# Performance work log

Measured on AMD Instinct MI355X. Metric: run time of the kernel, lower is better.

The kernel has to match this reference:

```python
import jax, jax.numpy as jnp
import numpy as np

D = 1024      # atrybuty (d_model)
H = 16        # kanaly (heads)
DH = D // H   # head dim
B, T = 4, 2048
EPS = 1e-5


def setup_inputs() -> dict:
    key = jax.random.key(0)
    ks = jax.random.split(key, 16)
    s = 0.02
    return {
        "x":  jax.random.normal(ks[0], (B, T, D), jnp.float32),
        "wq": jax.random.normal(ks[1], (D, D), jnp.float32) * s,
        "wk": jax.random.normal(ks[2], (D, D), jnp.float32) * s,
        "wv": jax.random.normal(ks[3], (D, D), jnp.float32) * s,
        "wp": jax.random.normal(ks[4], (D, D), jnp.float32) * s,
        "bp": jnp.zeros((D,), jnp.float32),
        "w1": jax.random.normal(ks[5], (D, 4 * D), jnp.float32) * s,
        "b1": jnp.zeros((4 * D,), jnp.float32),
        "w2": jax.random.normal(ks[6], (4 * D, D), jnp.float32) * s,
        "b2": jnp.zeros((D,), jnp.float32),
        "g1": jnp.ones((D,), jnp.float32),
        "be1": jnp.zeros((D,), jnp.float32),
        "g2": jnp.ones((D,), jnp.float32),
        "be2": jnp.zeros((D,), jnp.float32),
    }


def _layernorm(x, g, b):
    mu = jnp.mean(x, axis=-1, keepdims=True)
    var = jnp.mean(jnp.square(x - mu), axis=-1, keepdims=True)
    return (x - mu) * jax.lax.rsqrt(var + EPS) * g + b


def reference(x, wq, wk, wv, wp, bp, w1, b1, w2, b2, g1, be1, g2, be2):
    b, t, d = x.shape
    # --- self-attention on ln1(x) ---
    h = _layernorm(x, g1, be1)
    # per-head Linears are equivalent to one [D,D] projection split into heads
    q = (h @ wq).reshape(b, t, H, DH).transpose(0, 2, 1, 3)  # [B,H,T,Dh]
    k = (h @ wk).reshape(b, t, H, DH).transpose(0, 2, 1, 3)
    v = (h @ wv).reshape(b, t, H, DH).transpose(0, 2, 1, 3)
    # NOTE: original scales by full embed dim C, not head_dim
    scale = jnp.asarray(d, x.dtype) ** -0.5
    wei = jnp.einsum("bhqd,bhkd->bhqk", q, k) * scale
    causal = jnp.tril(jnp.ones((t, t), bool))
    wei = jnp.where(causal, wei, -jnp.inf)
    wei = jax.nn.softmax(wei, axis=-1)
    att = jnp.einsum("bhqk,bhkd->bhqd", wei, v)
    att = att.transpose(0, 2, 1, 3).reshape(b, t, d)
    x = x + att @ wp + bp
    # --- feedforward on ln2(x) ---
    h2 = _layernorm(x, g2, be2)
    x = x + jax.nn.relu(h2 @ w1 + b1) @ w2 + b2
    return x
```

## Files before the change

kernel.cpp:

```cpp
#include <hip/hip_runtime.h>
#include <hip/hip_bf16.h>
#include <stdint.h>

#define DM   1024
#define NH   16
#define DH   64
#define BATCH 4
#define SEQ  2048
#define MROWS (BATCH*SEQ)

typedef float f32x4 __attribute__((ext_vector_type(4)));
typedef __bf16 bf16x8 __attribute__((ext_vector_type(8)));
typedef short s16x4 __attribute__((ext_vector_type(4)));
typedef int   i32x2 __attribute__((ext_vector_type(2)));

#define QSCALE 0.045084220f

#define VM(n) asm volatile("s_waitcnt vmcnt(" #n ")" ::: "memory")
#define LGKM0 do { asm volatile("s_waitcnt lgkmcnt(0)" ::: "memory"); \
                   __builtin_amdgcn_sched_barrier(0); } while (0)

__device__ __forceinline__ short f2bs(float f) {
    __bf16 h = (__bf16)f;
    return __builtin_bit_cast(short, h);
}

__device__ __forceinline__ void gload_lds16(const void* g, void* l) {
    __builtin_amdgcn_global_load_lds(
        (__attribute__((address_space(1))) void*)(g),
        (__attribute__((address_space(3))) void*)(l), 16, 0, 0);
}

__device__ __forceinline__ void swz_xy(int ny, int& x, int& y) {
    const int bid = blockIdx.x;
    const int cpx = gridDim.x >> 3;
    const int wg  = (bid & 7) * cpx + (bid >> 3);
    x = wg / ny;
    y = wg % ny;
}

__global__ __launch_bounds__(256) void transpose_cvt_kernel(
    const float* __restrict__ w, short* __restrict__ wt, int K, int N)
{
    __shared__ short tile[64 * 65];
    const int k0 = blockIdx.x * 64, n0 = blockIdx.y * 64;
    const int t = threadIdx.x;
#pragma unroll
    for (int i = 0; i < 16; ++i) {
        int idx = i * 256 + t;
        int r = idx >> 6, c = idx & 63;
        tile[r * 65 + c] = f2bs(w[(size_t)(k0 + r) * N + n0 + c]);
    }
    __syncthreads();
#pragma unroll
    for (int i = 0; i < 16; ++i) {
        int idx = i * 256 + t;
        int r = idx >> 6, c = idx & 63;
        wt[(size_t)(n0 + r) * K + k0 + c] = tile[c * 65 + r];
    }
}

__global__ __launch_bounds__(256) void ln_kernel(
    const float* __restrict__ x, const float* __restrict__ g,
    const float* __restrict__ be, short* __restrict__ out)
{
    const int row = blockIdx.x, t = threadIdx.x;
    const float4 v = ((const float4*)(x + (size_t)row * DM))[t];
    float s  = v.x + v.y + v.z + v.w;
    float ss = v.x * v.x + v.y * v.y + v.z * v.z + v.w * v.w;
#pragma unroll
    for (int d = 1; d < 64; d <<= 1) {
        s  += __shfl_xor(s, d, 64);
        ss += __shfl_xor(ss, d, 64);
    }
    __shared__ float red[8];
    const int wid = t >> 6;
    if ((t & 63) == 0) { red[wid] = s; red[wid + 4] = ss; }
    __syncthreads();
    s  = red[0] + red[1] + red[2] + red[3];
    ss = red[4] + red[5] + red[6] + red[7];
    const float mu = s * (1.0f / DM);
    const float rs = rsqrtf(ss * (1.0f / DM) - mu * mu + 1e-5f);
    const float4 gg = ((const float4*)g)[t];
    const float4 bb = ((const float4*)be)[t];
    short4 o;
    o.x = f2bs((v.x - mu) * rs * gg.x + bb.x);
    o.y = f2bs((v.y - mu) * rs * gg.y + bb.y);
    o.z = f2bs((v.z - mu) * rs * gg.z + bb.z);
    o.w = f2bs((v.w - mu) * rs * gg.w + bb.w);
    ((short4*)(out + (size_t)row * DM))[t] = o;
}

template<int NCHUNK>
__device__ __forceinline__ void stage32(
    const short* __restrict__ G, int ldk, int row0, int k0,
    short* __restrict__ lds, int t)
{
#pragma unroll
    for (int i = 0; i < NCHUNK / 512; ++i) {
        const int c  = i * 512 + t;
        const int r  = c >> 2;
        const int sl = (c & 3) ^ ((r >> 1) & 3);
        gload_lds16(&G[(size_t)(row0 + r) * ldk + k0 + sl * 8], &lds[c * 8]);
    }
}

template<int EPI>
__global__ __launch_bounds__(512) void gemm256(
    const short* __restrict__ A, const short* __restrict__ Bt,
    int N, int K, int nyT,
    const float* __restrict__ bias, short* __restrict__ outb,
    short* __restrict__ qo, short* __restrict__ ko, short* __restrict__ vo)
{
    __shared__ short As[4][8192];
    __shared__ short Bs[4][8192];
    const int t = threadIdx.x, lane = t & 63, w = t >> 6;
    const int l15 = lane & 15, hi = lane >> 4;
    const int wm = (w >> 2) * 128, wn = (w & 3) * 64;
    int bx, by; swz_xy(nyT, bx, by);
    const int m0 = bx * 256, n0 = by * 256;
    const int NT = K >> 5;

    f32x4 acc[8][4] = {};

    stage32<1024>(A, K, m0, 0,  As[0], t); stage32<1024>(Bt, K, n0, 0,  Bs[0], t);
    stage32<1024>(A, K, m0, 32, As[1], t); stage32<1024>(Bt, K, n0, 32, Bs[1], t);
    stage32<1024>(A, K, m0, 64, As[2], t); stage32<1024>(Bt, K, n0, 64, Bs[2], t);
    VM(8);
    __builtin_amdgcn_s_barrier();

    for (int kt = 0; kt < NT; ++kt) {
        const short* Ac = As[kt & 3];
        const short* Bc = Bs[kt & 3];
        const int k3 = (kt + 3) << 5;
        bf16x8 af[8], bfr[4];

#pragma unroll
        for (int fm = 0; fm < 4; ++fm) {
            const int r = wm + fm * 16 + l15;
            af[fm] = *(const bf16x8*)&Ac[r * 32 + ((hi ^ ((r >> 1) & 3)) << 3)];
        }
#pragma unroll
        for (int fn = 0; fn < 4; ++fn) {
            const int r = wn + fn * 16 + l15;
            bfr[fn] = *(const bf16x8*)&Bc[r * 32 + ((hi ^ ((r >> 1) & 3)) << 3)];
        }
        if (kt + 3 < NT) stage32<1024>(A, K, m0, k3, As[(kt + 3) & 3], t);
        __builtin_amdgcn_s_barrier();
        LGKM0;
        __builtin_amdgcn_s_setprio(1);
#pragma unroll
        for (int fm = 0; fm < 4; ++fm)
#pragma unroll
            for (int fn = 0; fn < 4; ++fn)
                acc[fm][fn] = __builtin_amdgcn_mfma_f32_16x16x32_bf16(
                    af[fm], bfr[fn], acc[fm][fn], 0, 0, 0);
        __builtin_amdgcn_s_setprio(0);
        __builtin_amdgcn_s_barrier();

#pragma unroll
        for (int fm = 4; fm < 8; ++fm) {
            const int r = wm + fm * 16 + l15;
            af[fm] = *(const bf16x8*)&Ac[r * 32 + ((hi ^ ((r >> 1) & 3)) << 3)];
        }
        if (kt + 3 < NT) {
            stage32<1024>(Bt, K, n0, k3, Bs[(kt + 3) & 3], t);
            VM(8);
        } else if (kt + 2 < NT) VM(4);
        else if (kt + 1 < NT) VM(0);
        __builtin_amdgcn_s_barrier();
        LGKM0;
        __builtin_amdgcn_s_setprio(1);
#pragma unroll
        for (int fm = 4; fm < 8; ++fm)
#pragma unroll
            for (int fn = 0; fn < 4; ++fn)
                acc[fm][fn] = __builtin_amdgcn_mfma_f32_16x16x32_bf16(
                    af[fm], bfr[fn], acc[fm][fn], 0, 0, 0);
        __builtin_amdgcn_s_setprio(0);
        __builtin_amdgcn_s_barrier();
    }

#pragma unroll
    for (int fm = 0; fm < 8; ++fm)
#pragma unroll
        for (int fn = 0; fn < 4; ++fn) {
            const int row0 = m0 + wm + fm * 16 + hi * 4;
            const int nn = n0 + wn + fn * 16 + l15;
            const f32x4 a = acc[fm][fn];
            if constexpr (EPI == 0) {
                const int mat = nn >> 10, n1 = nn & 1023;
                const int head = n1 >> 6, dh = n1 & 63;
                if (mat == 2) {
                    const int tok = row0 & 2047, b = row0 >> 11;
                    const int tokp = (tok & ~63) |
                        (((((tok >> 3) & 7) ^ (dh & 7)) << 3)) | (tok & 7);
                    short4 pk;
                    pk.x = f2bs(a[0]); pk.y = f2bs(a[1]);
                    pk.z = f2bs(a[2]); pk.w = f2bs(a[3]);
                    *(short4*)&vo[((size_t)(b * NH + head) * DH + dh) * SEQ + tokp] = pk;
                } else if (mat == 1) {
#pragma unroll
                    for (int rr = 0; rr < 4; ++rr) {
                        const int m = row0 + rr;
                        const int b = m >> 11, tok = m & 2047;
                        const int dhp = (((dh >> 3) ^ (tok & 7)) << 3) | (dh & 7);
                        ko[((size_t)(b * NH + head) * SEQ + tok) * DH + dhp] =
                            f2bs(a[rr]);
                    }
                } else {
#pragma unroll
                    for (int rr = 0; rr < 4; ++rr) {
                        const int m = row0 + rr;
                        const int b = m >> 11, tok = m & 2047;
                        qo[((size_t)(b * NH + head) * SEQ + tok) * DH + dh] =
                            f2bs(a[rr] * QSCALE);
                    }
                }
            } else {
                const float bb = bias[nn];
#pragma unroll
                for (int rr = 0; rr < 4; ++rr) {
                    const float z = a[rr] + bb;
                    outb[(size_t)(row0 + rr) * N + nn] = f2bs(z > 0.f ? z : 0.f);
                }
            }
        }
}

__global__ __launch_bounds__(256) void gemm_bt128(
    const short* __restrict__ A, const short* __restrict__ Bt,
    int N, int K, int nyT,
    const float* __restrict__ bias, const float* __restrict__ res,
    float* __restrict__ outf)
{
    __shared__ short As[4][4096];
    __shared__ short Bs[4][4096];
    const int t = threadIdx.x, lane = t & 63, w = t >> 6;
    const int l15 = lane & 15, hi = lane >> 4;
    const int wm = (w & 1) * 64, wn = (w >> 1) * 64;
    int bx, by; swz_xy(nyT, bx, by);
    const int m0 = bx * 128, n0 = by * 128;
    const int NT = K >> 5;

    f32x4 acc[4][4] = {};

#define STAGE128(G, row0, k0, lds)                                            \
    do {                                                                      \
        _Pragma("unroll")                                                     \
        for (int i2 = 0; i2 < 2; ++i2) {                                      \
            const int c  = i2 * 256 + t;                                      \
            const int r  = c >> 2;                                            \
            const int sl = (c & 3) ^ ((r >> 1) & 3);                          \
            gload_lds16(&(G)[(size_t)((row0) + r) * K + (k0) + sl * 8],       \
                        &(lds)[c * 8]);                                       \
        }                                                                     \
    } while (0)

    STAGE128(A, m0, 0,  As[0]); STAGE128(Bt, n0, 0,  Bs[0]);
    STAGE128(A, m0, 32, As[1]); STAGE128(Bt, n0, 32, Bs[1]);
    STAGE128(A, m0, 64, As[2]); STAGE128(Bt, n0, 64, Bs[2]);

    for (int kt = 0; kt < NT; ++kt) {
        if (kt + 2 < NT) VM(8);
        else if (kt + 1 < NT) VM(4);
        else VM(0);
        __builtin_amdgcn_s_barrier();

        const short* Ac = As[kt & 3];
        const short* Bc = Bs[kt & 3];
        bf16x8 af[4], bfr[4];
#pragma unroll
        for (int fm = 0; fm < 4; ++fm) {
            const int r = wm + fm * 16 + l15;
            af[fm] = *(const bf16x8*)&Ac[r * 32 + ((hi ^ ((r >> 1) & 3)) << 3)];
        }
#pragma unroll
        for (int fn = 0; fn < 4; ++fn) {
            const int r = wn + fn * 16 + l15;
            bfr[fn] = *(const bf16x8*)&Bc[r * 32 + ((hi ^ ((r >> 1) & 3)) << 3)];
        }
#pragma unroll
        for (int fm = 0; fm < 4; ++fm)
#pragma unroll
            for (int fn = 0; fn < 4; ++fn)
                acc[fm][fn] = __builtin_amdgcn_mfma_f32_16x16x32_bf16(
                    af[fm], bfr[fn], acc[fm][fn], 0, 0, 0);

        __builtin_amdgcn_s_barrier();
        if (kt + 3 < NT) {
            STAGE128(A,  m0, (kt + 3) << 5, As[(kt + 3) & 3]);
            STAGE128(Bt, n0, (kt + 3) << 5, Bs[(kt + 3) & 3]);
        }
    }
#undef STAGE128

#pragma unroll
    for (int fm = 0; fm < 4; ++fm)
#pragma unroll
        for (int fn = 0; fn < 4; ++fn) {
            const int row0 = m0 + wm + fm * 16 + hi * 4;
            const int nn = n0 + wn + fn * 16 + l15;
            const float bb = bias[nn];
            const f32x4 a = acc[fm][fn];
#pragma unroll
            for (int rr = 0; rr < 4; ++rr) {
                const int m = row0 + rr;
                outf[(size_t)m * N + nn] = a[rr] + bb + res[(size_t)m * N + nn];
            }
        }
}

__global__ __launch_bounds__(512) void attn_kernel(
    const short* __restrict__ Q, const short* __restrict__ Kx,
    const short* __restrict__ Vt, short* __restrict__ att)
{
    __shared__ short Ks[2][4096];
    __shared__ short Vs[2][4096];

    const int n  = blockIdx.x;
    const int bh = n & 63;
    const int j  = n >> 6;
    const int qb = (j < 4) ? (7 - j) : (j - 4);
    const int tid = threadIdx.x;
    const int wq = tid >> 6;
    const int lane = tid & 63;
    const int l15 = lane & 15, hi = lane >> 4;
    const int qw = qb * 256 + wq * 32;
    const size_t base  = (size_t)bh * (SEQ * DH);
    const size_t vbase = (size_t)bh * (DH * SEQ);
    const int b = bh >> 4, head = bh & 15;

    bf16x8 qf[2][2];
#pragma unroll
    for (int mf = 0; mf < 2; ++mf)
#pragma unroll
        for (int kf = 0; kf < 2; ++kf)
            qf[mf][kf] = *(const bf16x8*)
                &Q[base + (size_t)(qw + mf * 16 + l15) * DH + kf * 32 + hi * 8];

    f32x4 O[2][4] = {};
    float L[2] = {0.f, 0.f};

    const int nkv_blk = 4 * qb + 4;
    const int nkv_wv  = (qw + 95) >> 6;

#define STAGE_KV(TT, BUF)                                                      \
    do {                                                                       \
        const int kvo = (TT) * 64;                                             \
        const int rw = tid >> 3, sl = tid & 7;                                 \
        gload_lds16(&Kx[base + (size_t)(kvo + rw) * DH + sl * 8],              \
                    &Ks[BUF][tid * 8]);                                        \
        gload_lds16(&Vt[vbase + (size_t)rw * SEQ + kvo + sl * 8],              \
                    &Vs[BUF][tid * 8]);                                        \
    } while (0)

    STAGE_KV(0, 0);

    for (int t2 = 0; t2 < nkv_blk; ++t2) {
        if (t2 + 1 < nkv_blk) { STAGE_KV(t2 + 1, (t2 + 1) & 1); VM(2); }
        else VM(0);
        __builtin_amdgcn_s_barrier();
        __builtin_amdgcn_sched_barrier(0);

        if (t2 < nkv_wv) {
            const short* Kc = Ks[t2 & 1];
            const short* Vc = Vs[t2 & 1];
            const int kv0 = t2 * 64;

            bf16x8 kfr[4][2];
#pragma unroll
            for (int nf = 0; nf < 4; ++nf)
#pragma unroll
                for (int kf = 0; kf < 2; ++kf)
                    kfr[nf][kf] = *(const bf16x8*)
                        &Kc[(nf * 16 + l15) * 64 + (((kf * 4 + hi) ^ (l15 & 7)) << 3)];

            f32x4 St[4][2] = {};
#pragma unroll
            for (int kf = 0; kf < 2; ++kf)
#pragma unroll
                for (int nf = 0; nf < 4; ++nf)
#pragma unroll
                    for (int mf = 0; mf < 2; ++mf)
                        St[nf][mf] = __builtin_amdgcn_mfma_f32_16x16x32_bf16(
                            kfr[nf][kf], qf[mf][kf], St[nf][mf], 0, 0, 0);

            if (kv0 + 63 > qw) {
#pragma unroll
                for (int mf = 0; mf < 2; ++mf) {
                    const int q = qw + mf * 16 + l15;
#pragma unroll
                    for (int nf = 0; nf < 4; ++nf)
#pragma unroll
                        for (int r = 0; r < 4; ++r) {
                            const int kv = kv0 + nf * 16 + hi * 4 + r;
                            if (kv > q) St[nf][mf][r] = -3.0e38f;
                        }
                }
            }

            s16x4 pa[4][2];
#pragma unroll
            for (int nf = 0; nf < 4; ++nf)
#pragma unroll
                for (int mf = 0; mf < 2; ++mf) {
                    const float p0 = exp2f(St[nf][mf][0]);
                    const float p1 = exp2f(St[nf][mf][1]);
                    const float p2 = exp2f(St[nf][mf][2]);
                    const float p3 = exp2f(St[nf][mf][3]);
                    L[mf] += (p0 + p1) + (p2 + p3);
                    unsigned dw0, dw1;
                    asm("v_cvt_pk_bf16_f32 %0, %1, %2" : "=v"(dw0) : "v"(p0), "v"(p1));
                    asm("v_cvt_pk_bf16_f32 %0, %1, %2" : "=v"(dw1) : "v"(p2), "v"(p3));
                    i32x2 dd; dd[0] = (int)dw0; dd[1] = (int)dw1;
                    pa[nf][mf] = __builtin_bit_cast(s16x4, dd);
                }

#pragma unroll
            for (int nf = 0; nf < 4; ++nf)
#pragma unroll
                for (int jf = 0; jf < 4; ++jf) {
                    const s16x4 vfr = *(const s16x4*)
                        &Vc[(jf * 16 + l15) * 64 +
                            ((((nf * 2 + (hi >> 1)) ^ (l15 & 7)) << 3) + ((hi & 1) << 2))];
#pragma unroll
                    for (int mf = 0; mf < 2; ++mf)
                        O[mf][jf] = __builtin_amdgcn_mfma_f32_16x16x16bf16_1k(
                            pa[nf][mf], vfr, O[mf][jf], 0, 0, 0);
                }
        }

        __builtin_amdgcn_sched_barrier(0);
        __builtin_amdgcn_s_barrier();
    }
#undef STAGE_KV

#pragma unroll
    for (int mf = 0; mf < 2; ++mf) {
        L[mf] += __shfl_xor(L[mf], 16, 64);
        L[mf] += __shfl_xor(L[mf], 32, 64);
    }
    const float inv0 = 1.0f / L[0], inv1 = 1.0f / L[1];

#pragma unroll
    for (int mf = 0; mf < 2; ++mf) {
        const float invm = mf ? inv1 : inv0;
#pragma unroll
        for (int r = 0; r < 4; ++r) {
            const int addr = ((lane >> 4) << 4) + (r << 2);
            const float iv = __builtin_bit_cast(float,
                __builtin_amdgcn_ds_bpermute(addr, __builtin_bit_cast(int, invm)));
            const int q = qw + mf * 16 + hi * 4 + r;
#pragma unroll
            for (int jf = 0; jf < 4; ++jf)
                att[(size_t)(b * SEQ + q) * DM + head * DH + jf * 16 + l15] =
                    f2bs(O[mf][jf][r] * iv);
        }
    }
}

extern "C" void kernel_launch(void* const* d_in, const int* in_sizes, int n_in,
                              void* d_out, int out_size, void* d_ws, size_t ws_size,
                              hipStream_t stream) {
    const float* x   = (const float*)d_in[0];
    const float* wq  = (const float*)d_in[1];
    const float* wk  = (const float*)d_in[2];
    const float* wv  = (const float*)d_in[3];
    const float* wp  = (const float*)d_in[4];
    const float* bp  = (const float*)d_in[5];
    const float* w1  = (const float*)d_in[6];
    const float* b1  = (const float*)d_in[7];
    const float* w2  = (const float*)d_in[8];
    const float* b2  = (const float*)d_in[9];
    const float* g1  = (const float*)d_in[10];
    const float* be1 = (const float*)d_in[11];
    const float* g2  = (const float*)d_in[12];
    const float* be2 = (const float*)d_in[13];
    float* out = (float*)d_out;

    char* ws = (char*)d_ws;
    short* wqkv_t = (short*)(ws + 0);
    short* wp_t   = (short*)(ws + 6291456);
    short* w1_t   = (short*)(ws + 8388608);
    short* w2_t   = (short*)(ws + 16777216);
    short* h      = (short*)(ws + 25165824);
    short* qb     = (short*)(ws + 41943040);
    short* kb     = (short*)(ws + 58720256);
    short* vb     = (short*)(ws + 75497472);
    short* att    = (short*)(ws + 92274688);
    float* x1     = (float*)(ws + 109051904);
    short* h2     = (short*)(ws + 142606336);
    short* tbuf   = (short*)(ws + 25165824);

    dim3 blk(256);

    transpose_cvt_kernel<<<dim3(16, 16), blk, 0, stream>>>(wq, wqkv_t,                1024, 1024);
    transpose_cvt_kernel<<<dim3(16, 16), blk, 0, stream>>>(wk, wqkv_t + 1024 * 1024,  1024, 1024);
    transpose_cvt_kernel<<<dim3(16, 16), blk, 0, stream>>>(wv, wqkv_t + 2048 * 1024,  1024, 1024);
    transpose_cvt_kernel<<<dim3(16, 16), blk, 0, stream>>>(wp, wp_t,                  1024, 1024);
    transpose_cvt_kernel<<<dim3(16, 64), blk, 0, stream>>>(w1, w1_t,                  1024, 4096);
    transpose_cvt_kernel<<<dim3(64, 16), blk, 0, stream>>>(w2, w2_t,                  4096, 1024);

    ln_kernel<<<MROWS, blk, 0, stream>>>(x, g1, be1, h);

    gemm256<0><<<dim3(384), dim3(512), 0, stream>>>(h, wqkv_t, 3072, 1024, 12,
        nullptr, nullptr, qb, kb, vb);

    attn_kernel<<<dim3(512), dim3(512), 0, stream>>>(qb, kb, vb, att);

    gemm_bt128<<<dim3(512), blk, 0, stream>>>(att, wp_t, 1024, 1024, 8,
        bp, x, x1);

    ln_kernel<<<MROWS, blk, 0, stream>>>(x1, g2, be2, h2);

    gemm256<2><<<dim3(512), dim3(512), 0, stream>>>(h2, w1_t, 4096, 1024, 16,
        b1, tbuf, nullptr, nullptr, nullptr);

    gemm_bt128<<<dim3(512), blk, 0, stream>>>(tbuf, w2_t, 1024, 4096, 8,
        b2, x1, out);
}
```

Baseline: 393.8 us.

## Stage two KV tiles per barrier in attention to halve synchronization

The attention loop now loads K/V in 128-row double tiles, each split into two 64-row sub-blocks, and processes both sub-blocks between barriers. This removes the trailing barrier per iteration and issues the next prefetch right after a single barrier, so there is half as many sync points per KV length. LDS use doubles to 64KB per block, which may lower occupancy. The VM(0) wait at the top of each iteration also gives up the finer-grained vmcnt overlap the old loop had. The row-sum accumulation now goes through a per-tile partial before being added to L.

```diff
diff --git a/kernel.cpp b/kernel.cpp
--- a/kernel.cpp
+++ b/kernel.cpp
@@ -315,16 +315,16 @@
     const short* __restrict__ Q, const short* __restrict__ Kx,
     const short* __restrict__ Vt, short* __restrict__ att)
 {
-    __shared__ short Ks[2][4096];
-    __shared__ short Vs[2][4096];
+    __shared__ short Ks[2][2][4096];
+    __shared__ short Vs[2][2][4096];
 
     const int n  = blockIdx.x;
     const int bh = n & 63;
     const int j  = n >> 6;
     const int qb = (j < 4) ? (7 - j) : (j - 4);
     const int tid = threadIdx.x;
+    const int lane = tid & 63;
     const int wq = tid >> 6;
-    const int lane = tid & 63;
     const int l15 = lane & 15, hi = lane >> 4;
     const int qw = qb * 256 + wq * 32;
     const size_t base  = (size_t)bh * (SEQ * DH);
@@ -343,29 +343,35 @@
     float L[2] = {0.f, 0.f};
 
     const int nkv_blk = 4 * qb + 4;
+    const int ndt     = nkv_blk >> 1;
     const int nkv_wv  = (qw + 95) >> 6;
 
-#define STAGE_KV(TT, BUF)                                                      \
+#define STAGE_KV2(DT, BUF)                                                     \
     do {                                                                       \
-        const int kvo = (TT) * 64;                                             \
+        const int kvo = (DT) * 128;                                            \
         const int rw = tid >> 3, sl = tid & 7;                                 \
-        gload_lds16(&Kx[base + (size_t)(kvo + rw) * DH + sl * 8],              \
-                    &Ks[BUF][tid * 8]);                                        \
-        gload_lds16(&Vt[vbase + (size_t)rw * SEQ + kvo + sl * 8],              \
-                    &Vs[BUF][tid * 8]);                                        \
+        _Pragma("unroll")                                                      \
+        for (int sb = 0; sb < 2; ++sb) {                                       \
+            gload_lds16(&Kx[base + (size_t)(kvo + sb * 64 + rw) * DH + sl * 8],\
+                        &Ks[BUF][sb][tid * 8]);                                \
+            gload_lds16(&Vt[vbase + (size_t)rw * SEQ + kvo + sb * 64 + sl * 8],\
+                        &Vs[BUF][sb][tid * 8]);                                \
+        }                                                                      \
     } while (0)
 
-    STAGE_KV(0, 0);
-
-    for (int t2 = 0; t2 < nkv_blk; ++t2) {
-        if (t2 + 1 < nkv_blk) { STAGE_KV(t2 + 1, (t2 + 1) & 1); VM(2); }
-        else VM(0);
-        __builtin_amdgcn_s_barrier();
-        __builtin_amdgcn_sched_barrier(0);
-
-        if (t2 < nkv_wv) {
-            const short* Kc = Ks[t2 & 1];
-            const short* Vc = Vs[t2 & 1];
+    STAGE_KV2(0, 0);
+
+    for (int dt = 0; dt < ndt; ++dt) {
+        VM(0);
+        __builtin_amdgcn_s_barrier();
+        if (dt + 1 < ndt) STAGE_KV2(dt + 1, (dt + 1) & 1);
+
+#pragma unroll
+        for (int sb = 0; sb < 2; ++sb) {
+            const int t2 = dt * 2 + sb;
+            if (t2 >= nkv_wv) break;
+            const short* Kc = &Ks[dt & 1][sb][0];
+            const short* Vc = &Vs[dt & 1][sb][0];
             const int kv0 = t2 * 64;
 
             bf16x8 kfr[4][2];
@@ -400,6 +406,7 @@
                 }
             }
 
+            float lp[2] = {0.f, 0.f};
             s16x4 pa[4][2];
 #pragma unroll
             for (int nf = 0; nf < 4; ++nf)
@@ -409,13 +416,14 @@
                     const float p1 = exp2f(St[nf][mf][1]);
                     const float p2 = exp2f(St[nf][mf][2]);
                     const float p3 = exp2f(St[nf][mf][3]);
-                    L[mf] += (p0 + p1) + (p2 + p3);
+                    lp[mf] += (p0 + p1) + (p2 + p3);
                     unsigned dw0, dw1;
                     asm("v_cvt_pk_bf16_f32 %0, %1, %2" : "=v"(dw0) : "v"(p0), "v"(p1));
                     asm("v_cvt_pk_bf16_f32 %0, %1, %2" : "=v"(dw1) : "v"(p2), "v"(p3));
                     i32x2 dd; dd[0] = (int)dw0; dd[1] = (int)dw1;
                     pa[nf][mf] = __builtin_bit_cast(s16x4, dd);
                 }
+            L[0] += lp[0]; L[1] += lp[1];
 
 #pragma unroll
             for (int nf = 0; nf < 4; ++nf)
@@ -430,11 +438,8 @@
                             pa[nf][mf], vfr, O[mf][jf], 0, 0, 0);
                 }
         }
-
-        __builtin_amdgcn_sched_barrier(0);
-        __builtin_amdgcn_s_barrier();
-    }
-#undef STAGE_KV
+    }
+#undef STAGE_KV2
 
 #pragma unroll
     for (int mf = 0; mf < 2; ++mf) {
```

New measurement: 383.0 us. -2.8%, faster.
